# Kernel tuning notes

Measured on AMD Instinct MI355X. Metric: run time of the kernel, lower is better.

## Reference

```python
import jax, jax.numpy as jnp
import numpy as np

DIM = 1024  # dim_model

def setup_inputs() -> dict:
    key = jax.random.key(0)
    ks = jax.random.split(key, 7)
    B, S, E = 4, 2048, 2 * DIM
    scale = 1.0 / np.sqrt(DIM)
    inputs = jax.random.normal(ks[0], (B, S, E), dtype=jnp.float32)
    Wq = jax.random.normal(ks[1], (DIM, DIM), dtype=jnp.float32) * scale
    bq = jax.random.normal(ks[2], (DIM,), dtype=jnp.float32) * 0.01
    Wk = jax.random.normal(ks[3], (DIM, DIM), dtype=jnp.float32) * scale
    bk = jax.random.normal(ks[4], (DIM,), dtype=jnp.float32) * 0.01
    Wv = jax.random.normal(ks[5], (DIM, DIM), dtype=jnp.float32) * scale
    bv = jax.random.normal(ks[6], (DIM,), dtype=jnp.float32) * 0.01
    return {"inputs": inputs, "Wq": Wq, "bq": bq, "Wk": Wk, "bk": bk, "Wv": Wv, "bv": bv}

def reference(inputs, Wq, bq, Wk, bk, Wv, bv):
    E = inputs.shape[-1]
    d = E // 2  # == dim_model
    vision_repr = inputs[:, :, :d]
    text_repr = inputs[:, :, d:]
    # torch nn.Linear: y = x @ W^T + b
    query = jnp.einsum('bsd,ed->bse', vision_repr, Wq) + bq
    key = jnp.einsum('bsd,ed->bse', text_repr, Wk) + bk
    value = jnp.einsum('bsd,ed->bse', text_repr, Wv) + bv
    scores = jnp.einsum('bqd,bkd->bqk', query, key) / jnp.sqrt(jnp.float32(d))
    attn = jax.nn.softmax(scores, axis=-1)  # [B, S, S]
    cross_attended_vision = jnp.einsum('bqk,bkd->bqd', attn, value)
    cross_attended_text = jnp.einsum('bqk,bqd->bkd', attn, vision_repr)
    return (cross_attended_vision, cross_attended_text)
```

## Files before the change

kernel.cpp:

```cpp
#include <hip/hip_runtime.h>

typedef unsigned short u16;
typedef unsigned int u32;
typedef __bf16 bf16x8 __attribute__((ext_vector_type(8)));
typedef float f32x4 __attribute__((ext_vector_type(4)));
typedef u16 u16x4 __attribute__((ext_vector_type(4)));
typedef u16 u16x8 __attribute__((ext_vector_type(8)));

__device__ __forceinline__ float b2f(u16 u) {
  union { float f; u32 i; } x; x.i = ((u32)u) << 16; return x.f;
}
__device__ __forceinline__ u16 f2b(float f) {
  union { float f; u32 i; } x; x.f = f;
  u32 r = (x.i + 0x7fffu + ((x.i >> 16) & 1u)) >> 16;
  return (u16)r;
}

__device__ __forceinline__ void gload16(const void* g, void* l) {
  __builtin_amdgcn_global_load_lds(
      (const __attribute__((address_space(1))) void*)g,
      (__attribute__((address_space(3))) void*)l, 16, 0, 0);
}


__global__ void convert_split(const float* __restrict__ in,
                              u16* __restrict__ vis, u16* __restrict__ txt) {
  size_t i = ((size_t)blockIdx.x * 256 + threadIdx.x) * 4;
  f32x4 v = *reinterpret_cast<const f32x4*>(in + i);
  size_t row = i >> 11;
  int col = (int)(i & 2047);
  u16x4 o = { f2b(v[0]), f2b(v[1]), f2b(v[2]), f2b(v[3]) };
  u16* dst = (col < 1024) ? (vis + row * 1024 + col)
                          : (txt + row * 1024 + (col - 1024));
  *reinterpret_cast<u16x4*>(dst) = o;
}

__global__ void convert_bf16(const float* __restrict__ in, u16* __restrict__ out) {
  size_t i = ((size_t)blockIdx.x * 256 + threadIdx.x) * 4;
  f32x4 v = *reinterpret_cast<const f32x4*>(in + i);
  u16x4 o = { f2b(v[0]), f2b(v[1]), f2b(v[2]), f2b(v[3]) };
  *reinterpret_cast<u16x4*>(out + i) = o;
}

__global__ void transpose_vision(const float* __restrict__ in, u16* __restrict__ out) {
  __shared__ float tile[64][65];
  const float* src = in + (size_t)blockIdx.z * (2048u * 2048u);
  u16* dst = out + (size_t)blockIdx.z * (1024u * 2048u);
  const int t = threadIdx.x;
  const int s0 = blockIdx.y * 64, d0 = blockIdx.x * 64;
#pragma unroll
  for (int p = 0; p < 16; ++p) {
    int idx = p * 256 + t; int r = idx >> 6, c = idx & 63;
    tile[r][c] = src[(size_t)(s0 + r) * 2048 + d0 + c];
  }
  __syncthreads();
#pragma unroll
  for (int p = 0; p < 16; ++p) {
    int idx = p * 256 + t; int r = idx >> 6, c = idx & 63;
    dst[(size_t)(d0 + r) * 2048 + s0 + c] = f2b(tile[c][r]);
  }
}

__global__ void transpose_bf16(const u16* __restrict__ in, u16* __restrict__ out,
                               int rows, int cols, long inB, long outB) {
  __shared__ u16 tile[64][65];
  const u16* src = in + (size_t)blockIdx.z * inB;
  u16* dst = out + (size_t)blockIdx.z * outB;
  const int t = threadIdx.x;
  const int r0 = blockIdx.y * 64, c0 = blockIdx.x * 64;
#pragma unroll
  for (int p = 0; p < 16; ++p) {
    int idx = p * 256 + t; int r = idx >> 6, c = idx & 63;
    tile[r][c] = src[(size_t)(r0 + r) * cols + c0 + c];
  }
  __syncthreads();
#pragma unroll
  for (int p = 0; p < 16; ++p) {
    int idx = p * 256 + t; int r = idx >> 6, c = idx & 63;
    dst[(size_t)(c0 + r) * rows + r0 + c] = tile[c][r];
  }
}

__launch_bounds__(256)
__global__ void softmax_kernel(u16* __restrict__ S) {
  __shared__ float red[8];
  u16* p = S + (size_t)blockIdx.x * 2048;
  const int t = threadIdx.x;
  u16x8 u = *reinterpret_cast<const u16x8*>(p + t * 8);
  float v[8];
#pragma unroll
  for (int j = 0; j < 8; ++j) v[j] = b2f(u[j]);
  float mx = v[0];
#pragma unroll
  for (int j = 1; j < 8; ++j) mx = fmaxf(mx, v[j]);
#pragma unroll
  for (int off = 32; off; off >>= 1) mx = fmaxf(mx, __shfl_xor(mx, off));
  if ((t & 63) == 0) red[t >> 6] = mx;
  __syncthreads();
  mx = fmaxf(fmaxf(red[0], red[1]), fmaxf(red[2], red[3]));
  float e[8], s = 0.f;
#pragma unroll
  for (int j = 0; j < 8; ++j) { e[j] = __expf(v[j] - mx); s += e[j]; }
#pragma unroll
  for (int off = 32; off; off >>= 1) s += __shfl_xor(s, off);
  if ((t & 63) == 0) red[4 + (t >> 6)] = s;
  __syncthreads();
  s = red[4] + red[5] + red[6] + red[7];
  const float inv = 1.0f / s;
  u16x8 o;
#pragma unroll
  for (int j = 0; j < 8; ++j) o[j] = f2b(e[j] * inv);
  *reinterpret_cast<u16x8*>(p + t * 8) = o;
}


struct GArgs {
  const u16* A[8]; const u16* B[8]; const float* bias[8]; void* C[8];
  int K, lda, ldb, ldc; float scale; int obf16;
};

#define FENCE() asm volatile("" ::: "memory")
#define BARF()  { FENCE(); __builtin_amdgcn_s_barrier(); FENCE(); }
#define LGKM0() { asm volatile("s_waitcnt lgkmcnt(0)" ::: "memory"); __builtin_amdgcn_sched_barrier(0); }
#define LGKM8() asm volatile("s_waitcnt lgkmcnt(8)" ::: "memory")
#define VMC4()  asm volatile("s_waitcnt vmcnt(4)" ::: "memory")
#define PRIO1() __builtin_amdgcn_s_setprio(1)
#define PRIO0() { __builtin_amdgcn_s_setprio(0); __builtin_amdgcn_sched_barrier(0); }

__launch_bounds__(512, 2)
__global__ void gemm256(GArgs args) {
  __shared__ u16 lds[65536];
  char* L = (char*)lds;
  const int t = threadIdx.x;
  const int z = blockIdx.z;
  const u16* A  = args.A[z];
  const u16* Bm = args.B[z];
  const int K = args.K, lda = args.lda, ldb = args.ldb, ldc = args.ldc;
  const int bm = blockIdx.y, bn = blockIdx.x;
  const int lane = t & 63, wave = t >> 6;
  const int wr = (wave >> 2) * 128;
  const int wc = (wave & 3) * 64;
  const int fr = lane & 15, kh = lane >> 4;
  const int sw = (fr & 7) << 4;
  const u32 cK0 = (u32)((kh << 4) ^ sw);
  const u32 cK1 = (u32)((64 | (kh << 4)) ^ sw);
  const u32 offA = (u32)((wr ? 16384 : 0) + fr * 128);
  const u32 offB = (u32)(32768 + ((wc & 128) ? 16384 : 0) + ((wc & 64) ? 8192 : 0) + fr * 128);
  const int srow = t >> 3;
  const int scol = ((((t & 7) << 4) ^ (((t >> 3) & 7) << 4)) >> 1);
  const u32 sdst = (u32)(t * 16);
  const u16* Ab = A  + (size_t)(bm * 256 + srow) * lda + scol;
  const u16* Bb = Bm + (size_t)(bn * 256 + srow) * ldb + scol;

  f32x4 acc[8][4];
  const f32x4 zero = {0.f, 0.f, 0.f, 0.f};
#pragma unroll
  for (int a = 0; a < 8; ++a)
#pragma unroll
    for (int n = 0; n < 4; ++n) acc[a][n] = zero;

  bf16x8 af[4][2], bg0[2][2], bg1[2][2];

  auto STAGE_A = [&](int bufOff, int half, int k0) {
    const u16* s = Ab + (size_t)(half * 128) * lda + k0;
    char* d = L + bufOff + half * 16384 + sdst;
    gload16(s, d);
    gload16(s + (size_t)64 * lda, d + 8192);
  };
  auto STAGE_B = [&](int bufOff, int half, int k0) {
    const u16* s = Bb + (size_t)(half * 128) * ldb + k0;
    char* d = L + bufOff + 32768 + half * 16384 + sdst;
    gload16(s, d);
    gload16(s + (size_t)64 * ldb, d + 8192);
  };
  auto LDA = [&](int bufOff, int h) {
#pragma unroll
    for (int mi = 0; mi < 4; ++mi) {
      u32 base = (u32)bufOff + offA + (u32)(h * 8192 + mi * 2048);
      af[mi][0] = *reinterpret_cast<const bf16x8*>(L + base + cK0);
      af[mi][1] = *reinterpret_cast<const bf16x8*>(L + base + cK1);
    }
  };
  auto LDB = [&](int bufOff, int g, bf16x8 (&bg)[2][2]) {
#pragma unroll
    for (int ni = 0; ni < 2; ++ni) {
      u32 base = (u32)bufOff + offB + (u32)(g * 4096 + ni * 2048);
      bg[ni][0] = *reinterpret_cast<const bf16x8*>(L + base + cK0);
      bg[ni][1] = *reinterpret_cast<const bf16x8*>(L + base + cK1);
    }
  };
  auto MF = [&](int h, int g, bf16x8 (&bg)[2][2]) {
#pragma unroll
    for (int mi = 0; mi < 4; ++mi)
#pragma unroll
      for (int ni = 0; ni < 2; ++ni)
#pragma unroll
        for (int kk = 0; kk < 2; ++kk)
          acc[h * 4 + mi][g * 2 + ni] = __builtin_amdgcn_mfma_f32_16x16x32_bf16(
              af[mi][kk], bg[ni][kk], acc[h * 4 + mi][g * 2 + ni], 0, 0, 0);
  };

  STAGE_A(0, 0, 0); STAGE_A(0, 1, 0); STAGE_B(0, 0, 0); STAGE_B(0, 1, 0);
  STAGE_B(65536, 0, 64); STAGE_B(65536, 1, 64);
  VMC4();
  BARF();

  const int nIter = K >> 7;
  for (int it = 0; it < nIter; ++it) {
    const int tt = it * 2;
    const int k1 = (tt + 1) << 6;
    int k2 = (tt + 2) << 6; if (k2 >= K) k2 = 0;
    int k3 = (tt + 3) << 6; if (k3 >= K) k3 = 0;
    LDA(0, 0); LDB(0, 0, bg0);
    STAGE_A(65536, 0, k1);
    LGKM8();
    BARF(); LGKM0();
    PRIO1(); MF(0, 0, bg0); PRIO0();
    BARF();
    LDB(0, 1, bg1);
    STAGE_A(65536, 1, k1);
    BARF(); LGKM0();
    PRIO1(); MF(0, 1, bg1); PRIO0();
    BARF();
    LDA(0, 1);
    STAGE_B(0, 0, k2);
    BARF(); LGKM0();
    PRIO1(); MF(1, 1, bg1); PRIO0();
    BARF();
    STAGE_B(0, 1, k2);
    BARF();
    PRIO1(); MF(1, 0, bg0); PRIO0();
    VMC4();
    BARF();
    LDA(65536, 0); LDB(65536, 0, bg0);
    STAGE_A(0, 0, k2);
    LGKM8();
    BARF(); LGKM0();
    PRIO1(); MF(0, 0, bg0); PRIO0();
    BARF();
    LDB(65536, 1, bg1);
    STAGE_A(0, 1, k2);
    BARF(); LGKM0();
    PRIO1(); MF(0, 1, bg1); PRIO0();
    BARF();
    LDA(65536, 1);
    STAGE_B(65536, 0, k3);
    BARF(); LGKM0();
    PRIO1(); MF(1, 1, bg1); PRIO0();
    BARF();
    STAGE_B(65536, 1, k3);
    BARF();
    PRIO1(); MF(1, 0, bg0); PRIO0();
    VMC4();
    BARF();
  }

  const float scl = args.scale;
  const float* bias = args.bias[z];
  float bv[4];
#pragma unroll
  for (int ni = 0; ni < 4; ++ni) {
    int n = bn * 256 + wc + ni * 16 + fr;
    bv[ni] = bias ? bias[n] : 0.f;
  }
  if (args.obf16) {
    u16* C = (u16*)args.C[z];
#pragma unroll
    for (int a = 0; a < 8; ++a) {
      const int mb = bm * 256 + wr + (a >> 2) * 64 + (a & 3) * 16 + kh * 4;
#pragma unroll
      for (int ni = 0; ni < 4; ++ni) {
        const int n = bn * 256 + wc + ni * 16 + fr;
#pragma unroll
        for (int r = 0; r < 4; ++r)
          C[(size_t)(mb + r) * ldc + n] = f2b(acc[a][ni][r] * scl + bv[ni]);
      }
    }
  } else {
    float* C = (float*)args.C[z];
#pragma unroll
    for (int a = 0; a < 8; ++a) {
      const int mb = bm * 256 + wr + (a >> 2) * 64 + (a & 3) * 16 + kh * 4;
#pragma unroll
      for (int ni = 0; ni < 4; ++ni) {
        const int n = bn * 256 + wc + ni * 16 + fr;
#pragma unroll
        for (int r = 0; r < 4; ++r)
          C[(size_t)(mb + r) * ldc + n] = acc[a][ni][r] * scl + bv[ni];
      }
    }
  }
}

extern "C" void kernel_launch(void* const* d_in, const int* in_sizes, int n_in,
                              void* d_out, int out_size, void* d_ws, size_t ws_size,
                              hipStream_t stream) {
  const float* inp = (const float*)d_in[0];
  const float* Wq  = (const float*)d_in[1];
  const float* bq  = (const float*)d_in[2];
  const float* Wk  = (const float*)d_in[3];
  const float* bk  = (const float*)d_in[4];
  const float* Wv  = (const float*)d_in[5];
  const float* bv  = (const float*)d_in[6];
  float* out = (float*)d_out;
  char* ws = (char*)d_ws;

  u16* visB  = (u16*)(ws + 0);
  u16* textB = (u16*)(ws + 16777216);
  u16* Vtmp  = (u16*)(ws + 0);
  u16* Sattn = (u16*)(ws + 0);
  u16* visT  = (u16*)(ws + 33554432);
  u16* WqB   = (u16*)(ws + 50331648);
  u16* WkB   = (u16*)(ws + 52428800);
  u16* WvB   = (u16*)(ws + 54525952);
  u16* Qb    = (u16*)(ws + 56623104);
  u16* Kb    = (u16*)(ws + 73400320);
  u16* attnT = (u16*)(ws + 56623104);
  u16* Vt    = (u16*)(ws + 90177536);

  convert_split<<<16384, 256, 0, stream>>>(inp, visB, textB);
  convert_bf16<<<1024, 256, 0, stream>>>(Wq, WqB);
  convert_bf16<<<1024, 256, 0, stream>>>(Wk, WkB);
  convert_bf16<<<1024, 256, 0, stream>>>(Wv, WvB);
  transpose_vision<<<dim3(16, 32, 4), 256, 0, stream>>>(inp, visT);

  {
    GArgs g{};
    g.A[0] = visB;  g.B[0] = WqB; g.bias[0] = bq; g.C[0] = Qb;
    g.A[1] = textB; g.B[1] = WkB; g.bias[1] = bk; g.C[1] = Kb;
    g.A[2] = textB; g.B[2] = WvB; g.bias[2] = bv; g.C[2] = Vtmp;
    g.K = 1024; g.lda = 1024; g.ldb = 1024; g.ldc = 1024; g.scale = 1.f; g.obf16 = 1;
    gemm256<<<dim3(4, 32, 3), 512, 0, stream>>>(g);
  }

  transpose_bf16<<<dim3(16, 32, 4), 256, 0, stream>>>(Vtmp, Vt, 2048, 1024, 2048L * 1024, 1024L * 2048);

  {
    GArgs g{};
    for (int z = 0; z < 4; ++z) {
      g.A[z] = Qb + (size_t)z * 2097152;
      g.B[z] = Kb + (size_t)z * 2097152;
      g.bias[z] = nullptr;
      g.C[z] = Sattn + (size_t)z * 4194304;
    }
    g.K = 1024; g.lda = 1024; g.ldb = 1024; g.ldc = 2048; g.scale = 0.03125f; g.obf16 = 1;
    gemm256<<<dim3(8, 8, 4), 512, 0, stream>>>(g);
  }

  softmax_kernel<<<8192, 256, 0, stream>>>(Sattn);

  transpose_bf16<<<dim3(32, 32, 4), 256, 0, stream>>>(Sattn, attnT, 2048, 2048, 4194304L, 4194304L);

  {
    GArgs g{};
    for (int z = 0; z < 4; ++z) {
      g.A[z] = Sattn + (size_t)z * 4194304;
      g.B[z] = Vt + (size_t)z * 2097152;
      g.bias[z] = nullptr;
      g.C[z] = out + (size_t)z * 2097152;
    }
    for (int z = 4; z < 8; ++z) {
      g.A[z] = attnT + (size_t)(z - 4) * 4194304;
      g.B[z] = visT + (size_t)(z - 4) * 2097152;
      g.bias[z] = nullptr;
      g.C[z] = out + 8388608 + (size_t)(z - 4) * 2097152;
    }
    g.K = 2048; g.lda = 2048; g.ldb = 2048; g.ldc = 1024; g.scale = 1.f; g.obf16 = 0;
    gemm256<<<dim3(4, 8, 8), 512, 0, stream>>>(g);
  }
}
```

Baseline: 338.1 us.

## Fuse input conversion with transpose, swizzle GEMM blocks, coalesce epilogue via LDS

Merges the input split/convert and vision transpose into one kernel that reads the fp32 input once, and merges the three weight conversions into one launch. The GEMM remaps block indices across XCD-sized chunks for better L2 locality. Its epilogue stages results through LDS so global stores are wide and coalesced. The V projection moves to its own launch after Q/K, which avoids Vtmp overwriting visB while the Q GEMM still reads it, at the cost of one more launch and a less full grid.

Measured after the change: 336.9 us. Within noise of the previous version (-0.4%).

```diff
diff --git a/kernel.cpp b/kernel.cpp
--- a/kernel.cpp
+++ b/kernel.cpp
@@ -22,43 +22,48 @@
       (__attribute__((address_space(3))) void*)l, 16, 0, 0);
 }
 
-
-__global__ void convert_split(const float* __restrict__ in,
-                              u16* __restrict__ vis, u16* __restrict__ txt) {
+__global__ void convert_all(const float* __restrict__ in, u16* __restrict__ vis,
+                            u16* __restrict__ txt, u16* __restrict__ visT) {
+  __shared__ float tile[64][65];
+  const int t = threadIdx.x;
+  const int e0 = blockIdx.x * 64;
+  const int s0 = blockIdx.y * 64;
+  const bool isVis = e0 < 1024;
+  u16* dst = isVis ? vis : txt;
+  const int ec = isVis ? e0 : (e0 - 1024);
+#pragma unroll
+  for (int p = 0; p < 4; ++p) {
+    int idx = p * 256 + t; int r = idx >> 4; int c4 = (idx & 15) << 2;
+    f32x4 v = *reinterpret_cast<const f32x4*>(&in[(size_t)(s0 + r) * 2048 + e0 + c4]);
+    u16x4 o = { f2b(v[0]), f2b(v[1]), f2b(v[2]), f2b(v[3]) };
+    *reinterpret_cast<u16x4*>(&dst[(size_t)(s0 + r) * 1024 + ec + c4]) = o;
+    if (isVis) {
+      tile[r][c4] = v[0]; tile[r][c4 + 1] = v[1];
+      tile[r][c4 + 2] = v[2]; tile[r][c4 + 3] = v[3];
+    }
+  }
+  if (!isVis) return;
+  __syncthreads();
+  const int b = s0 >> 11, sl = s0 & 2047;
+#pragma unroll
+  for (int p = 0; p < 4; ++p) {
+    int idx = p * 256 + t; int r = idx >> 4; int c4 = (idx & 15) << 2;
+    u16x4 o = { f2b(tile[c4][r]), f2b(tile[c4 + 1][r]),
+                f2b(tile[c4 + 2][r]), f2b(tile[c4 + 3][r]) };
+    *reinterpret_cast<u16x4*>(
+        &visT[(size_t)b * 2097152 + (size_t)(e0 + r) * 2048 + sl + c4]) = o;
+  }
+}
+
+__global__ void convert_w(const float* __restrict__ a, const float* __restrict__ b,
+                          const float* __restrict__ c, u16* __restrict__ oa,
+                          u16* __restrict__ ob, u16* __restrict__ oc) {
+  const float* src = blockIdx.y == 0 ? a : (blockIdx.y == 1 ? b : c);
+  u16* dst = blockIdx.y == 0 ? oa : (blockIdx.y == 1 ? ob : oc);
   size_t i = ((size_t)blockIdx.x * 256 + threadIdx.x) * 4;
-  f32x4 v = *reinterpret_cast<const f32x4*>(in + i);
-  size_t row = i >> 11;
-  int col = (int)(i & 2047);
+  f32x4 v = *reinterpret_cast<const f32x4*>(src + i);
   u16x4 o = { f2b(v[0]), f2b(v[1]), f2b(v[2]), f2b(v[3]) };
-  u16* dst = (col < 1024) ? (vis + row * 1024 + col)
-                          : (txt + row * 1024 + (col - 1024));
-  *reinterpret_cast<u16x4*>(dst) = o;
-}
-
-__global__ void convert_bf16(const float* __restrict__ in, u16* __restrict__ out) {
-  size_t i = ((size_t)blockIdx.x * 256 + threadIdx.x) * 4;
-  f32x4 v = *reinterpret_cast<const f32x4*>(in + i);
-  u16x4 o = { f2b(v[0]), f2b(v[1]), f2b(v[2]), f2b(v[3]) };
-  *reinterpret_cast<u16x4*>(out + i) = o;
-}
-
-__global__ void transpose_vision(const float* __restrict__ in, u16* __restrict__ out) {
-  __shared__ float tile[64][65];
-  const float* src = in + (size_t)blockIdx.z * (2048u * 2048u);
-  u16* dst = out + (size_t)blockIdx.z * (1024u * 2048u);
-  const int t = threadIdx.x;
-  const int s0 = blockIdx.y * 64, d0 = blockIdx.x * 64;
-#pragma unroll
-  for (int p = 0; p < 16; ++p) {
-    int idx = p * 256 + t; int r = idx >> 6, c = idx & 63;
-    tile[r][c] = src[(size_t)(s0 + r) * 2048 + d0 + c];
-  }
-  __syncthreads();
-#pragma unroll
-  for (int p = 0; p < 16; ++p) {
-    int idx = p * 256 + t; int r = idx >> 6, c = idx & 63;
-    dst[(size_t)(d0 + r) * 2048 + s0 + c] = f2b(tile[c][r]);
-  }
+  *reinterpret_cast<u16x4*>(dst + i) = o;
 }
 
 __global__ void transpose_bf16(const u16* __restrict__ in, u16* __restrict__ out,
@@ -113,7 +118,6 @@
   *reinterpret_cast<u16x8*>(p + t * 8) = o;
 }
 
-
 struct GArgs {
   const u16* A[8]; const u16* B[8]; const float* bias[8]; void* C[8];
   int K, lda, ldb, ldc; float scale; int obf16;
@@ -124,6 +128,7 @@
 #define LGKM0() { asm volatile("s_waitcnt lgkmcnt(0)" ::: "memory"); __builtin_amdgcn_sched_barrier(0); }
 #define LGKM8() asm volatile("s_waitcnt lgkmcnt(8)" ::: "memory")
 #define VMC4()  asm volatile("s_waitcnt vmcnt(4)" ::: "memory")
+#define VMC0()  asm volatile("s_waitcnt vmcnt(0)" ::: "memory")
 #define PRIO1() __builtin_amdgcn_s_setprio(1)
 #define PRIO0() { __builtin_amdgcn_s_setprio(0); __builtin_amdgcn_sched_barrier(0); }
 
@@ -132,11 +137,26 @@
   __shared__ u16 lds[65536];
   char* L = (char*)lds;
   const int t = threadIdx.x;
-  const int z = blockIdx.z;
+
+  const int nx = gridDim.x, ny = gridDim.y;
+  int bn, bm, z;
+  {
+    int lin = blockIdx.x + nx * (blockIdx.y + ny * blockIdx.z);
+    const int tot = nx * ny * (int)gridDim.z;
+    if (!(tot & 7)) {
+      const int chunk = tot >> 3;
+      lin = (lin & 7) * chunk + (lin >> 3);
+    }
+    const int nxy = nx * ny;
+    z = lin / nxy;
+    const int rr = lin - z * nxy;
+    bm = rr / nx;
+    bn = rr - bm * nx;
+  }
+
   const u16* A  = args.A[z];
   const u16* Bm = args.B[z];
   const int K = args.K, lda = args.lda, ldb = args.ldb, ldc = args.ldc;
-  const int bm = blockIdx.y, bn = blockIdx.x;
   const int lane = t & 63, wave = t >> 6;
   const int wr = (wave >> 2) * 128;
   const int wc = (wave & 3) * 64;
@@ -255,6 +275,9 @@
     BARF();
   }
 
+  VMC0();
+  __syncthreads();
+
   const float scl = args.scale;
   const float* bias = args.bias[z];
   float bv[4];
@@ -263,31 +286,63 @@
     int n = bn * 256 + wc + ni * 16 + fr;
     bv[ni] = bias ? bias[n] : 0.f;
   }
+  const int wh = wave >> 2;
+
   if (args.obf16) {
     u16* C = (u16*)args.C[z];
-#pragma unroll
-    for (int a = 0; a < 8; ++a) {
-      const int mb = bm * 256 + wr + (a >> 2) * 64 + (a & 3) * 16 + kh * 4;
-#pragma unroll
-      for (int ni = 0; ni < 4; ++ni) {
-        const int n = bn * 256 + wc + ni * 16 + fr;
-#pragma unroll
-        for (int r = 0; r < 4; ++r)
-          C[(size_t)(mb + r) * ldc + n] = f2b(acc[a][ni][r] * scl + bv[ni]);
+    u16* LH = (u16*)lds;
+#pragma unroll
+    for (int h = 0; h < 2; ++h) {
+      if (wh == h) {
+#pragma unroll
+        for (int a = 0; a < 8; ++a) {
+          const int rb = (a >> 2) * 64 + (a & 3) * 16 + kh * 4;
+#pragma unroll
+          for (int ni = 0; ni < 4; ++ni) {
+            const int col = wc + ni * 16 + fr;
+#pragma unroll
+            for (int r = 0; r < 4; ++r)
+              LH[(rb + r) * 256 + col] = f2b(acc[a][ni][r] * scl + bv[ni]);
+          }
+        }
       }
+      __syncthreads();
+#pragma unroll
+      for (int i = 0; i < 8; ++i) {
+        int idx = i * 512 + t; int row = idx >> 5; int c8 = (idx & 31) << 3;
+        *reinterpret_cast<u16x8*>(
+            &C[(size_t)(bm * 256 + h * 128 + row) * ldc + bn * 256 + c8]) =
+            *reinterpret_cast<const u16x8*>(&LH[row * 256 + c8]);
+      }
+      __syncthreads();
     }
   } else {
     float* C = (float*)args.C[z];
-#pragma unroll
-    for (int a = 0; a < 8; ++a) {
-      const int mb = bm * 256 + wr + (a >> 2) * 64 + (a & 3) * 16 + kh * 4;
-#pragma unroll
-      for (int ni = 0; ni < 4; ++ni) {
-        const int n = bn * 256 + wc + ni * 16 + fr;
-#pragma unroll
-        for (int r = 0; r < 4; ++r)
-          C[(size_t)(mb + r) * ldc + n] = acc[a][ni][r] * scl + bv[ni];
+    float* LF = (float*)lds;
+#pragma unroll
+    for (int h = 0; h < 2; ++h) {
+      if (wh == h) {
+#pragma unroll
+        for (int a = 0; a < 8; ++a) {
+          const int rb = (a >> 2) * 64 + (a & 3) * 16 + kh * 4;
+#pragma unroll
+          for (int ni = 0; ni < 4; ++ni) {
+            const int col = wc + ni * 16 + fr;
+#pragma unroll
+            for (int r = 0; r < 4; ++r)
+              LF[(rb + r) * 256 + col] = acc[a][ni][r] * scl + bv[ni];
+          }
+        }
       }
+      __syncthreads();
+#pragma unroll
+      for (int i = 0; i < 16; ++i) {
+        int idx = i * 512 + t; int row = idx >> 6; int c4 = (idx & 63) << 2;
+        *reinterpret_cast<f32x4*>(
+            &C[(size_t)(bm * 256 + h * 128 + row) * ldc + bn * 256 + c4]) =
+            *reinterpret_cast<const f32x4*>(&LF[row * 256 + c4]);
+      }
+      __syncthreads();
     }
   }
 }
@@ -318,19 +373,21 @@
   u16* attnT = (u16*)(ws + 56623104);
   u16* Vt    = (u16*)(ws + 90177536);
 
-  convert_split<<<16384, 256, 0, stream>>>(inp, visB, textB);
-  convert_bf16<<<1024, 256, 0, stream>>>(Wq, WqB);
-  convert_bf16<<<1024, 256, 0, stream>>>(Wk, WkB);
-  convert_bf16<<<1024, 256, 0, stream>>>(Wv, WvB);
-  transpose_vision<<<dim3(16, 32, 4), 256, 0, stream>>>(inp, visT);
+  convert_all<<<dim3(32, 128), 256, 0, stream>>>(inp, visB, textB, visT);
+  convert_w<<<dim3(1024, 3), 256, 0, stream>>>(Wq, Wk, Wv, WqB, WkB, WvB);
 
   {
     GArgs g{};
     g.A[0] = visB;  g.B[0] = WqB; g.bias[0] = bq; g.C[0] = Qb;
     g.A[1] = textB; g.B[1] = WkB; g.bias[1] = bk; g.C[1] = Kb;
-    g.A[2] = textB; g.B[2] = WvB; g.bias[2] = bv; g.C[2] = Vtmp;
     g.K = 1024; g.lda = 1024; g.ldb = 1024; g.ldc = 1024; g.scale = 1.f; g.obf16 = 1;
-    gemm256<<<dim3(4, 32, 3), 512, 0, stream>>>(g);
+    gemm256<<<dim3(4, 32, 2), 512, 0, stream>>>(g);
+  }
+  {
+    GArgs g{};
+    g.A[0] = textB; g.B[0] = WvB; g.bias[0] = bv; g.C[0] = Vtmp;
+    g.K = 1024; g.lda = 1024; g.ldb = 1024; g.ldc = 1024; g.scale = 1.f; g.obf16 = 1;
+    gemm256<<<dim3(4, 32, 1), 512, 0, stream>>>(g);
   }
 
   transpose_bf16<<<dim3(16, 32, 4), 256, 0, stream>>>(Vtmp, Vt, 2048, 1024, 2048L * 1024, 1024L * 2048);
```
